# Kernel tuning notes

Measured on AMD Instinct MI355X. Metric: run time of the kernel, lower is better.

The kernel has to match this reference:

```python
import jax, jax.numpy as jnp
import numpy as np

N = 4_194_304
EPS = 1e-7
ACLIP = 1.0 - 1e-6  # keep arccos away from +/-1 so gradients stay finite


def _circle_giou(x, y):
    # x, y: [N, 3] = (center_row, center_col, radius). shapely's
    # Point(row, col).buffer(rad) is a disk; we use the exact closed forms
    # for disk-disk intersection and the convex hull of two disks.
    cx0, cy0, r0 = x[:, 0], x[:, 1], x[:, 2]
    cx1, cy1, r1 = y[:, 0], y[:, 1], y[:, 2]
    PI = jnp.float32(np.pi)

    d2 = (cx0 - cx1) ** 2 + (cy0 - cy1) ** 2
    d = jnp.sqrt(jnp.maximum(d2, EPS))
    rmax = jnp.maximum(r0, r1)
    rmin = jnp.minimum(r0, r1)

    # --- intersection area (lens formula with branch masks) ---
    lens = (d < r0 + r1) & (d > rmax - rmin)
    contained = d <= rmax - rmin
    cos0 = jnp.clip((d2 + r0 * r0 - r1 * r1) / jnp.maximum(2.0 * d * r0, EPS), -ACLIP, ACLIP)
    cos1 = jnp.clip((d2 + r1 * r1 - r0 * r0) / jnp.maximum(2.0 * d * r1, EPS), -ACLIP, ACLIP)
    t = (r0 + r1 - d) * (d + r0 - r1) * (d - r0 + r1) * (d + r0 + r1)
    t_safe = jnp.where(lens, jnp.maximum(t, EPS), 1.0)  # keep sqrt grad finite off-branch
    lens_area = r0 * r0 * jnp.arccos(cos0) + r1 * r1 * jnp.arccos(cos1) - 0.5 * jnp.sqrt(t_safe)
    inter = jnp.where(lens, lens_area, jnp.where(contained, PI * rmin * rmin, 0.0))

    union = PI * (r0 * r0 + r1 * r1) - inter
    iou = inter / jnp.maximum(union, EPS)

    # --- convex hull of the two disks ---
    # Non-contained case: two arcs + two external tangent trapezoids.
    # alpha = angle from center line to tangent point, cos(alpha) = (rmax-rmin)/d
    alpha = jnp.arccos(jnp.clip((rmax - rmin) / d, 0.0, ACLIP))
    h2 = d2 - (rmax - rmin) ** 2
    h2_safe = jnp.where(contained, 1.0, jnp.maximum(h2, EPS))
    hull_open = (rmax * rmax * (PI - alpha) + rmin * rmin * alpha
                 + (rmax + rmin) * jnp.sqrt(h2_safe))
    hull = jnp.where(contained, PI * rmax * rmax, hull_open)

    # giou loss per pair: 1 - (IoU - (hull - union)/hull)
    return 1.0 - (iou - (hull - union) / jnp.maximum(hull, EPS))


def setup_inputs() -> dict:
    key = jax.random.key(0)
    k1, k2 = jax.random.split(key)
    x = jax.random.uniform(k1, (N, 3), dtype=jnp.float32)
    y = jax.random.uniform(k2, (N, 3), dtype=jnp.float32)
    return {"x": x, "y": y}


def reference(x, y):
    # GIOULOSS.forward: sum over per-pair GIoU losses -> scalar
    return jnp.sum(_circle_giou(x, y))
```

## Files before the change

kernel.cpp:

```cpp
#include <hip/hip_runtime.h>
#include <math.h>


#define EPSF   1e-07f
#define ACLIPF (1.0f - 1e-06f)
#define PIF    3.14159265358979323846f

__device__ __forceinline__ float frcp(float x)  { return __builtin_amdgcn_rcpf(x); }
__device__ __forceinline__ float fsqrt(float x) { return __builtin_amdgcn_sqrtf(x); }

__device__ __forceinline__ float fast_acos(float x) {
    float ax = fabsf(x);
    float p = fmaf(fmaf(fmaf(-0.0187293f, ax, 0.0742610f), ax, -0.2121144f), ax, 1.5707288f);
    float r = fsqrt(1.0f - ax) * p;
    return x < 0.0f ? PIF - r : r;
}

__device__ __forceinline__ float circle_giou(float cx0, float cy0, float r0,
                                             float cx1, float cy1, float r1) {
    float dx = cx0 - cx1, dy = cy0 - cy1;
    float d2 = fmaf(dx, dx, dy * dy);
    float d  = fsqrt(fmaxf(d2, EPSF));
    float rmax = fmaxf(r0, r1), rmin = fminf(r0, r1);
    float rdiff = rmax - rmin, rsum = r0 + r1;
    bool lens      = (d < rsum) && (d > rdiff);
    bool contained = (d <= rdiff);

    float r0s = r0 * r0, r1s = r1 * r1;
    float inv0 = frcp(fmaxf(2.0f * d * r0, EPSF));
    float inv1 = frcp(fmaxf(2.0f * d * r1, EPSF));
    float cos0 = fminf(fmaxf((d2 + r0s - r1s) * inv0, -ACLIPF), ACLIPF);
    float cos1 = fminf(fmaxf((d2 + r1s - r0s) * inv1, -ACLIPF), ACLIPF);

    float t = (rsum * rsum - d2) * (d2 - rdiff * rdiff);
    float t_safe = lens ? fmaxf(t, EPSF) : 1.0f;
    float lens_area = r0s * fast_acos(cos0) + r1s * fast_acos(cos1) - 0.5f * fsqrt(t_safe);
    float inter = lens ? lens_area : (contained ? PIF * rmin * rmin : 0.0f);
    float uni = PIF * (r0s + r1s) - inter;
    float iou = inter * frcp(fmaxf(uni, EPSF));

    float alpha = fast_acos(fminf(rdiff * frcp(d), ACLIPF));
    float h2 = d2 - rdiff * rdiff;
    float h2_safe = contained ? 1.0f : fmaxf(h2, EPSF);
    float hull_open = rmax * rmax * (PIF - alpha) + rmin * rmin * alpha
                      + (rmax + rmin) * fsqrt(h2_safe);
    float hull = contained ? PIF * rmax * rmax : hull_open;

    return 1.0f - (iou - (hull - uni) * frcp(fmaxf(hull, EPSF)));
}

__device__ __forceinline__ float giou4(float4 xa, float4 xb, float4 xc,
                                       float4 ya, float4 yb, float4 yc) {
    float s = 0.0f;
    s += circle_giou(xa.x, xa.y, xa.z,  ya.x, ya.y, ya.z);
    s += circle_giou(xa.w, xb.x, xb.y,  ya.w, yb.x, yb.y);
    s += circle_giou(xb.z, xb.w, xc.x,  yb.z, yb.w, yc.x);
    s += circle_giou(xc.y, xc.z, xc.w,  yc.y, yc.z, yc.w);
    return s;
}

__global__ __launch_bounds__(256)
void GIOULOSS_19524921327670_stage1(const float4* __restrict__ x4,
                                    const float4* __restrict__ y4,
                                    float* __restrict__ partial, int nthreads) {
    int t = blockIdx.x * blockDim.x + threadIdx.x;
    int g0 = t, g1 = t + nthreads;

    float4 xa0 = x4[3 * g0 + 0], xb0 = x4[3 * g0 + 1], xc0 = x4[3 * g0 + 2];
    float4 ya0 = y4[3 * g0 + 0], yb0 = y4[3 * g0 + 1], yc0 = y4[3 * g0 + 2];
    float4 xa1 = x4[3 * g1 + 0], xb1 = x4[3 * g1 + 1], xc1 = x4[3 * g1 + 2];
    float4 ya1 = y4[3 * g1 + 0], yb1 = y4[3 * g1 + 1], yc1 = y4[3 * g1 + 2];

    float acc = giou4(xa0, xb0, xc0, ya0, yb0, yc0)
              + giou4(xa1, xb1, xc1, ya1, yb1, yc1);

    #pragma unroll
    for (int off = 32; off > 0; off >>= 1)
        acc += __shfl_down(acc, off, 64);

    __shared__ float wave_sums[4];
    int lane = threadIdx.x & 63;
    int wave = threadIdx.x >> 6;
    if (lane == 0) wave_sums[wave] = acc;
    __syncthreads();
    if (threadIdx.x == 0)
        partial[blockIdx.x] = wave_sums[0] + wave_sums[1] + wave_sums[2] + wave_sums[3];
}

__global__ __launch_bounds__(256)
void GIOULOSS_19524921327670_stage2(const float* __restrict__ partial,
                                    float* __restrict__ out) {
    const float4* p4 = (const float4*)partial;
    float4 a = p4[threadIdx.x];
    float4 b = p4[threadIdx.x + 256];
    float acc = (a.x + a.y) + (a.z + a.w) + (b.x + b.y) + (b.z + b.w);

    #pragma unroll
    for (int off = 32; off > 0; off >>= 1)
        acc += __shfl_down(acc, off, 64);

    __shared__ float wave_sums[4];
    int lane = threadIdx.x & 63;
    int wave = threadIdx.x >> 6;
    if (lane == 0) wave_sums[wave] = acc;
    __syncthreads();
    if (threadIdx.x == 0)
        out[0] = wave_sums[0] + wave_sums[1] + wave_sums[2] + wave_sums[3];
}

extern "C" void kernel_launch(void* const* d_in, const int* in_sizes, int n_in,
                              void* d_out, int out_size, void* d_ws, size_t ws_size,
                              hipStream_t stream) {
    const float4* x4 = (const float4*)d_in[0];
    const float4* y4 = (const float4*)d_in[1];
    float* out = (float*)d_out;
    float* partial = (float*)d_ws;

    int n = in_sizes[0] / 3;
    int ngroups = n / 4;
    int nthreads = ngroups / 2;
    int block = 256;
    int grid = nthreads / block;

    GIOULOSS_19524921327670_stage1<<<grid, block, 0, stream>>>(x4, y4, partial, nthreads);
    GIOULOSS_19524921327670_stage2<<<1, block, 0, stream>>>(partial, out);
}
```

Before: 115.5 us.

## Stage coalesced input loads through LDS with register prefetch across batches

Each block now processes four batches of 768 float4 per input, loading them with fully coalesced accesses into shared memory and prefetching the next batch into registers while the current one is computed. This replaces the previous strided per-thread float4 loads and halves the grid, with stage two reduced to match the 1024 partials. The costs are extra LDS traffic, synchronisation, possible bank conflicts on the stride-12 reads, and a grid size hardcoded to the problem size.

```diff
diff --git a/kernel.cpp b/kernel.cpp
--- a/kernel.cpp
+++ b/kernel.cpp
@@ -59,20 +59,42 @@
     return s;
 }
 
+#define NBATCH 4
+
 __global__ __launch_bounds__(256)
 void GIOULOSS_19524921327670_stage1(const float4* __restrict__ x4,
                                     const float4* __restrict__ y4,
-                                    float* __restrict__ partial, int nthreads) {
-    int t = blockIdx.x * blockDim.x + threadIdx.x;
-    int g0 = t, g1 = t + nthreads;
+                                    float* __restrict__ partial) {
+    __shared__ float4 bufx[768];
+    __shared__ float4 bufy[768];
 
-    float4 xa0 = x4[3 * g0 + 0], xb0 = x4[3 * g0 + 1], xc0 = x4[3 * g0 + 2];
-    float4 ya0 = y4[3 * g0 + 0], yb0 = y4[3 * g0 + 1], yc0 = y4[3 * g0 + 2];
-    float4 xa1 = x4[3 * g1 + 0], xb1 = x4[3 * g1 + 1], xc1 = x4[3 * g1 + 2];
-    float4 ya1 = y4[3 * g1 + 0], yb1 = y4[3 * g1 + 1], yc1 = y4[3 * g1 + 2];
+    const int t = threadIdx.x;
+    const int b = blockIdx.x;
 
-    float acc = giou4(xa0, xb0, xc0, ya0, yb0, yc0)
-              + giou4(xa1, xb1, xc1, ya1, yb1, yc1);
+    int base = (b * NBATCH + 0) * 768;
+    float4 gx0 = x4[base + t], gx1 = x4[base + 256 + t], gx2 = x4[base + 512 + t];
+    float4 gy0 = y4[base + t], gy1 = y4[base + 256 + t], gy2 = y4[base + 512 + t];
+
+    float acc = 0.0f;
+    #pragma unroll
+    for (int i = 0; i < NBATCH; ++i) {
+        __syncthreads();
+        bufx[t] = gx0; bufx[256 + t] = gx1; bufx[512 + t] = gx2;
+        bufy[t] = gy0; bufy[256 + t] = gy1; bufy[512 + t] = gy2;
+
+        if (i + 1 < NBATCH) {
+            int nb = (b * NBATCH + i + 1) * 768;
+            gx0 = x4[nb + t]; gx1 = x4[nb + 256 + t]; gx2 = x4[nb + 512 + t];
+            gy0 = y4[nb + t]; gy1 = y4[nb + 256 + t]; gy2 = y4[nb + 512 + t];
+        }
+        __syncthreads();
+
+        const float4* px = (const float4*)((const float*)bufx + 12 * t);
+        const float4* py = (const float4*)((const float*)bufy + 12 * t);
+        float4 xa = px[0], xb = px[1], xc = px[2];
+        float4 ya = py[0], yb = py[1], yc = py[2];
+        acc += giou4(xa, xb, xc, ya, yb, yc);
+    }
 
     #pragma unroll
     for (int off = 32; off > 0; off >>= 1)
@@ -92,8 +114,7 @@
                                     float* __restrict__ out) {
     const float4* p4 = (const float4*)partial;
     float4 a = p4[threadIdx.x];
-    float4 b = p4[threadIdx.x + 256];
-    float acc = (a.x + a.y) + (a.z + a.w) + (b.x + b.y) + (b.z + b.w);
+    float acc = (a.x + a.y) + (a.z + a.w);
 
     #pragma unroll
     for (int off = 32; off > 0; off >>= 1)
@@ -116,12 +137,9 @@
     float* out = (float*)d_out;
     float* partial = (float*)d_ws;
 
-    int n = in_sizes[0] / 3;
-    int ngroups = n / 4;
-    int nthreads = ngroups / 2;
     int block = 256;
-    int grid = nthreads / block;
+    int grid = 1024;
 
-    GIOULOSS_19524921327670_stage1<<<grid, block, 0, stream>>>(x4, y4, partial, nthreads);
+    GIOULOSS_19524921327670_stage1<<<grid, block, 0, stream>>>(x4, y4, partial);
     GIOULOSS_19524921327670_stage2<<<1, block, 0, stream>>>(partial, out);
 }
```

New measurement: 116.8 us. No clear change (+1.1%).
